# Kernel optimization log

Hardware: AMD Instinct MI355X
Metric: run time of the kernel (lower is better)

Reference implementation:

```python
import jax, jax.numpy as jnp
import numpy as np

DIM = 256
MUL = 4
NUM_ENTRIES = 64
B, K = 16, 64
R = MUL * DIM


def setup_inputs() -> dict:
    key = jax.random.key(0)
    k_slots, k_idx, k_w1, k_w2 = jax.random.split(key, 4)
    slots = jax.random.normal(k_slots, (B, K, DIM), dtype=jnp.float32)
    indices = jax.random.randint(k_idx, (B, K), 0, NUM_ENTRIES, dtype=jnp.int64)
    # xavier_normal: std = sqrt(2 / (fan_in + fan_out)) over last two dims
    std1 = float(np.sqrt(2.0 / (DIM + R)))
    std2 = float(np.sqrt(2.0 / (R + DIM)))
    w1 = jax.random.normal(k_w1, (NUM_ENTRIES, DIM, R), dtype=jnp.float32) * std1
    w2 = jax.random.normal(k_w2, (NUM_ENTRIES, R, DIM), dtype=jnp.float32) * std2
    b1 = jnp.zeros((NUM_ENTRIES, R), dtype=jnp.float32)
    b2 = jnp.zeros((NUM_ENTRIES, DIM), dtype=jnp.float32)
    return {"slots": slots, "w1": w1, "b1": b1, "w2": w2, "b2": b2, "indices": indices}


def reference(slots, w1, b1, w2, b2, indices):
    # gather per-(b,k) expert weights, then 2-layer MLP (matvec per slot)
    h = jnp.einsum('bkd,bkdr->bkr', slots, w1[indices]) + b1[indices]  # (B,K,R)
    h = jax.nn.relu(h)
    out = jnp.einsum('bkr,bkrd->bkd', h, w2[indices]) + b2[indices]    # (B,K,DIM)
    return out
```

## Files before the change

kernel.cpp:

```cpp
#include <hip/hip_runtime.h>
#include <stdint.h>

#define DIMC 256
#define RTOT 1024
#define NE 64
#define NSLOT 1024
#define RC 256
#define TILE 32
#define XSTR 264
#define KS 8
#define NTW 4

typedef short bfrag __attribute__((ext_vector_type(8)));
typedef float f32x4 __attribute__((ext_vector_type(4)));

__global__ __launch_bounds__(1024) void bucket_kernel(
    const int* __restrict__ idx, int* __restrict__ count,
    int* __restrict__ start, int* __restrict__ list) {
  __shared__ int cnt[NE];
  __shared__ int offs[NE];
  __shared__ int cur[NE];
  int t = threadIdx.x;
  if (t < NE) cnt[t] = 0;
  __syncthreads();
  int e = idx[t] & (NE - 1);
  atomicAdd(&cnt[e], 1);
  __syncthreads();
  if (t == 0) {
    int acc = 0;
    for (int i = 0; i < NE; ++i) { offs[i] = acc; cur[i] = acc; acc += cnt[i]; }
  }
  __syncthreads();
  if (t < NE) { count[t] = cnt[t]; start[t] = offs[t]; }
  int pos = atomicAdd(&cur[e], 1);
  list[pos] = t;
}

static __device__ __forceinline__ unsigned short f2bf(float f) {
  unsigned u = __float_as_uint(f);
  return (unsigned short)((u + 0x7FFFu + ((u >> 16) & 1u)) >> 16);
}

static __device__ __forceinline__ bfrag pack8(const float* f) {
  union { unsigned short u[8]; bfrag v; } r;
#pragma unroll
  for (int i = 0; i < 8; ++i) r.u[i] = f2bf(f[i]);
  return r.v;
}

__global__ __launch_bounds__(256) void mlp_kernel(
    const float* __restrict__ slots, const float* __restrict__ w1,
    const float* __restrict__ b1, const float* __restrict__ w2,
    const float* __restrict__ b2, const int* __restrict__ count,
    const int* __restrict__ start, const int* __restrict__ list,
    float* __restrict__ out) {
  const int rc = blockIdx.x;
  const int e  = blockIdx.y;
  const int n  = count[e];
  if (n == 0) return;
  const int t  = threadIdx.x;
  const int l  = t & 63;
  const int w  = t >> 6;
  const int ln = l & 15;
  const int kg = l >> 4;
  const int rbase = rc * RC;
  const int n0 = w * 64;
  const int st = start[e];

  __shared__ unsigned short X[TILE * XSTR];
  __shared__ int sid[TILE];

  const float* w1e = w1 + (size_t)e * DIMC * RTOT + rbase;
  const float* w2e = w2 + (size_t)e * RTOT * DIMC + (size_t)rbase * DIMC;

  for (int s0 = 0; s0 < n; s0 += TILE) {
    const int m = (n - s0 < TILE) ? (n - s0) : TILE;

    __syncthreads();
    if (t < TILE) sid[t] = (t < m) ? list[st + s0 + t] : 0;
    __syncthreads();

    for (int i = t; i < TILE * 64; i += 256) {
      int s = i >> 6, d4 = (i & 63) * 4;
      float4 v = make_float4(0.f, 0.f, 0.f, 0.f);
      if (s < m) v = ((const float4*)slots)[(size_t)sid[s] * 64 + (i & 63)];
      union { unsigned short u[4]; uint2 q; } p;
      p.u[0] = f2bf(v.x); p.u[1] = f2bf(v.y);
      p.u[2] = f2bf(v.z); p.u[3] = f2bf(v.w);
      *(uint2*)&X[s * XSTR + d4] = p.q;
    }
    __syncthreads();

    f32x4 acc[2][NTW];
#pragma unroll
    for (int mt = 0; mt < 2; ++mt)
#pragma unroll
      for (int nt = 0; nt < NTW; ++nt) acc[mt][nt] = (f32x4)(0.f);

    {
      float bc[NTW][8], bn[NTW][8];
#pragma unroll
      for (int nt = 0; nt < NTW; ++nt)
#pragma unroll
        for (int j = 0; j < 8; ++j)
          bc[nt][j] = w1e[(size_t)(kg * 8 + j) * RTOT + n0 + nt * 16 + ln];

#pragma unroll
      for (int ks = 0; ks < KS; ++ks) {
        if (ks + 1 < KS) {
          const int kb = (ks + 1) * 32;
#pragma unroll
          for (int nt = 0; nt < NTW; ++nt)
#pragma unroll
            for (int j = 0; j < 8; ++j)
              bn[nt][j] = w1e[(size_t)(kb + kg * 8 + j) * RTOT + n0 + nt * 16 + ln];
        }
        const unsigned short* xp = &X[(size_t)ln * XSTR + ks * 32 + kg * 8];
        bfrag a0 = *(const bfrag*)xp;
        bfrag a1 = *(const bfrag*)(xp + 16 * XSTR);
#pragma unroll
        for (int nt = 0; nt < NTW; ++nt) {
          bfrag b = pack8(bc[nt]);
          acc[0][nt] = __builtin_amdgcn_mfma_f32_16x16x32_bf16(a0, b, acc[0][nt], 0, 0, 0);
          acc[1][nt] = __builtin_amdgcn_mfma_f32_16x16x32_bf16(a1, b, acc[1][nt], 0, 0, 0);
        }
#pragma unroll
        for (int nt = 0; nt < NTW; ++nt)
#pragma unroll
          for (int j = 0; j < 8; ++j) bc[nt][j] = bn[nt][j];
      }
    }

    __syncthreads();

#pragma unroll
    for (int nt = 0; nt < NTW; ++nt) {
      const int col = n0 + nt * 16 + ln;
      const float b1v = b1[e * RTOT + rbase + col];
#pragma unroll
      for (int mt = 0; mt < 2; ++mt) {
#pragma unroll
        for (int reg = 0; reg < 4; ++reg) {
          float h = fmaxf(acc[mt][nt][reg] + b1v, 0.f);
          X[(mt * 16 + kg * 4 + reg) * XSTR + col] = f2bf(h);
        }
        acc[mt][nt] = (f32x4)(0.f);
      }
    }
    __syncthreads();

    {
      float bc[NTW][8], bn[NTW][8];
#pragma unroll
      for (int nt = 0; nt < NTW; ++nt)
#pragma unroll
        for (int j = 0; j < 8; ++j)
          bc[nt][j] = w2e[(size_t)(kg * 8 + j) * DIMC + n0 + nt * 16 + ln];

#pragma unroll
      for (int ks = 0; ks < KS; ++ks) {
        if (ks + 1 < KS) {
          const int kb = (ks + 1) * 32;
#pragma unroll
          for (int nt = 0; nt < NTW; ++nt)
#pragma unroll
            for (int j = 0; j < 8; ++j)
              bn[nt][j] = w2e[(size_t)(kb + kg * 8 + j) * DIMC + n0 + nt * 16 + ln];
        }
        const unsigned short* xp = &X[(size_t)ln * XSTR + ks * 32 + kg * 8];
        bfrag a0 = *(const bfrag*)xp;
        bfrag a1 = *(const bfrag*)(xp + 16 * XSTR);
#pragma unroll
        for (int nt = 0; nt < NTW; ++nt) {
          bfrag b = pack8(bc[nt]);
          acc[0][nt] = __builtin_amdgcn_mfma_f32_16x16x32_bf16(a0, b, acc[0][nt], 0, 0, 0);
          acc[1][nt] = __builtin_amdgcn_mfma_f32_16x16x32_bf16(a1, b, acc[1][nt], 0, 0, 0);
        }
#pragma unroll
        for (int nt = 0; nt < NTW; ++nt)
#pragma unroll
          for (int j = 0; j < 8; ++j) bc[nt][j] = bn[nt][j];
      }
    }

#pragma unroll
    for (int nt = 0; nt < NTW; ++nt) {
      const int col = n0 + nt * 16 + ln;
      const float b2v = (rc == 0) ? b2[e * DIMC + col] : 0.f;
#pragma unroll
      for (int mt = 0; mt < 2; ++mt)
#pragma unroll
        for (int reg = 0; reg < 4; ++reg) {
          const int row = mt * 16 + kg * 4 + reg;
          if (row < m)
            atomicAdd(&out[(size_t)sid[row] * DIMC + col], acc[mt][nt][reg] + b2v);
        }
    }
  }
}

extern "C" void kernel_launch(void* const* d_in, const int* in_sizes, int n_in,
                              void* d_out, int out_size, void* d_ws, size_t ws_size,
                              hipStream_t stream) {
  const float* slots   = (const float*)d_in[0];
  const float* w1      = (const float*)d_in[1];
  const float* b1      = (const float*)d_in[2];
  const float* w2      = (const float*)d_in[3];
  const float* b2      = (const float*)d_in[4];
  const int*   indices = (const int*)d_in[5];
  float* out = (float*)d_out;

  int* ws    = (int*)d_ws;
  int* count = ws;
  int* start = ws + 64;
  int* list  = ws + 128;

  hipMemsetAsync(d_out, 0, (size_t)out_size * sizeof(float), stream);
  bucket_kernel<<<1, NSLOT, 0, stream>>>(indices, count, start, list);
  mlp_kernel<<<dim3(4, NE), 256, 0, stream>>>(slots, w1, b1, w2, b2,
                                              count, start, list, out);
}
```

Measured before the change: 179.4 us.

## Split hidden dim into 8 chunks with 512-thread blocks for more parallelism

The hidden dimension is now split into 8 chunks of 128 instead of 4 chunks of 256, and each block uses 8 waves instead of 4. In the first GEMM each wave now owns one 16-column tile. In the second GEMM each wave owns 32 output columns and reduces over 128 hidden rows. This doubles the grid and the waves per block to raise occupancy and memory-level parallelism on the weight streaming, which appears to be the bottleneck. In exchange it doubles the atomicAdd traffic into the output and makes each block reload the slot tile twice as often.

```diff
diff --git a/kernel.cpp b/kernel.cpp
--- a/kernel.cpp
+++ b/kernel.cpp
@@ -5,11 +5,13 @@
 #define RTOT 1024
 #define NE 64
 #define NSLOT 1024
-#define RC 256
+#define RCN 8
+#define RCW 128
 #define TILE 32
 #define XSTR 264
-#define KS 8
-#define NTW 4
+#define KS1 8
+#define KS2 4
+#define NTW2 2
 
 typedef short bfrag __attribute__((ext_vector_type(8)));
 typedef float f32x4 __attribute__((ext_vector_type(4)));
@@ -48,7 +50,7 @@
   return r.v;
 }
 
-__global__ __launch_bounds__(256) void mlp_kernel(
+__global__ __launch_bounds__(512) void mlp_kernel(
     const float* __restrict__ slots, const float* __restrict__ w1,
     const float* __restrict__ b1, const float* __restrict__ w2,
     const float* __restrict__ b2, const int* __restrict__ count,
@@ -63,8 +65,7 @@
   const int w  = t >> 6;
   const int ln = l & 15;
   const int kg = l >> 4;
-  const int rbase = rc * RC;
-  const int n0 = w * 64;
+  const int rbase = rc * RCW;
   const int st = start[e];
 
   __shared__ unsigned short X[TILE * XSTR];
@@ -80,7 +81,7 @@
     if (t < TILE) sid[t] = (t < m) ? list[st + s0 + t] : 0;
     __syncthreads();
 
-    for (int i = t; i < TILE * 64; i += 256) {
+    for (int i = t; i < TILE * 64; i += 512) {
       int s = i >> 6, d4 = (i & 63) * 4;
       float4 v = make_float4(0.f, 0.f, 0.f, 0.f);
       if (s < m) v = ((const float4*)slots)[(size_t)sid[s] * 64 + (i & 63)];
@@ -91,101 +92,91 @@
     }
     __syncthreads();
 
-    f32x4 acc[2][NTW];
-#pragma unroll
-    for (int mt = 0; mt < 2; ++mt)
-#pragma unroll
-      for (int nt = 0; nt < NTW; ++nt) acc[mt][nt] = (f32x4)(0.f);
-
+    f32x4 acc1[2];
+    acc1[0] = (f32x4)(0.f); acc1[1] = (f32x4)(0.f);
     {
-      float bc[NTW][8], bn[NTW][8];
-#pragma unroll
-      for (int nt = 0; nt < NTW; ++nt)
-#pragma unroll
-        for (int j = 0; j < 8; ++j)
-          bc[nt][j] = w1e[(size_t)(kg * 8 + j) * RTOT + n0 + nt * 16 + ln];
-
-#pragma unroll
-      for (int ks = 0; ks < KS; ++ks) {
-        if (ks + 1 < KS) {
+      const int col = w * 16 + ln;
+      float bc[8], bn[8];
+#pragma unroll
+      for (int j = 0; j < 8; ++j)
+        bc[j] = w1e[(size_t)(kg * 8 + j) * RTOT + col];
+
+#pragma unroll
+      for (int ks = 0; ks < KS1; ++ks) {
+        if (ks + 1 < KS1) {
           const int kb = (ks + 1) * 32;
 #pragma unroll
-          for (int nt = 0; nt < NTW; ++nt)
-#pragma unroll
-            for (int j = 0; j < 8; ++j)
-              bn[nt][j] = w1e[(size_t)(kb + kg * 8 + j) * RTOT + n0 + nt * 16 + ln];
+          for (int j = 0; j < 8; ++j)
+            bn[j] = w1e[(size_t)(kb + kg * 8 + j) * RTOT + col];
         }
         const unsigned short* xp = &X[(size_t)ln * XSTR + ks * 32 + kg * 8];
         bfrag a0 = *(const bfrag*)xp;
         bfrag a1 = *(const bfrag*)(xp + 16 * XSTR);
-#pragma unroll
-        for (int nt = 0; nt < NTW; ++nt) {
-          bfrag b = pack8(bc[nt]);
-          acc[0][nt] = __builtin_amdgcn_mfma_f32_16x16x32_bf16(a0, b, acc[0][nt], 0, 0, 0);
-          acc[1][nt] = __builtin_amdgcn_mfma_f32_16x16x32_bf16(a1, b, acc[1][nt], 0, 0, 0);
-        }
-#pragma unroll
-        for (int nt = 0; nt < NTW; ++nt)
-#pragma unroll
-          for (int j = 0; j < 8; ++j) bc[nt][j] = bn[nt][j];
+        bfrag b = pack8(bc);
+        acc1[0] = __builtin_amdgcn_mfma_f32_16x16x32_bf16(a0, b, acc1[0], 0, 0, 0);
+        acc1[1] = __builtin_amdgcn_mfma_f32_16x16x32_bf16(a1, b, acc1[1], 0, 0, 0);
+#pragma unroll
+        for (int j = 0; j < 8; ++j) bc[j] = bn[j];
       }
     }
 
     __syncthreads();
 
-#pragma unroll
-    for (int nt = 0; nt < NTW; ++nt) {
-      const int col = n0 + nt * 16 + ln;
+    {
+      const int col = w * 16 + ln;
       const float b1v = b1[e * RTOT + rbase + col];
 #pragma unroll
-      for (int mt = 0; mt < 2; ++mt) {
+      for (int mt = 0; mt < 2; ++mt)
 #pragma unroll
         for (int reg = 0; reg < 4; ++reg) {
-          float h = fmaxf(acc[mt][nt][reg] + b1v, 0.f);
+          float h = fmaxf(acc1[mt][reg] + b1v, 0.f);
           X[(mt * 16 + kg * 4 + reg) * XSTR + col] = f2bf(h);
         }
-        acc[mt][nt] = (f32x4)(0.f);
-      }
-    }
-    __syncthreads();
-
+    }
+    __syncthreads();
+
+    f32x4 acc2[2][NTW2];
+#pragma unroll
+    for (int mt = 0; mt < 2; ++mt)
+#pragma unroll
+      for (int nt = 0; nt < NTW2; ++nt) acc2[mt][nt] = (f32x4)(0.f);
     {
-      float bc[NTW][8], bn[NTW][8];
-#pragma unroll
-      for (int nt = 0; nt < NTW; ++nt)
+      float bc[NTW2][8], bn[NTW2][8];
+#pragma unroll
+      for (int nt = 0; nt < NTW2; ++nt)
 #pragma unroll
         for (int j = 0; j < 8; ++j)
-          bc[nt][j] = w2e[(size_t)(kg * 8 + j) * DIMC + n0 + nt * 16 + ln];
-
-#pragma unroll
-      for (int ks = 0; ks < KS; ++ks) {
-        if (ks + 1 < KS) {
+          bc[nt][j] = w2e[(size_t)(kg * 8 + j) * DIMC + w * 32 + nt * 16 + ln];
+
+#pragma unroll
+      for (int ks = 0; ks < KS2; ++ks) {
+        if (ks + 1 < KS2) {
           const int kb = (ks + 1) * 32;
 #pragma unroll
-          for (int nt = 0; nt < NTW; ++nt)
+          for (int nt = 0; nt < NTW2; ++nt)
 #pragma unroll
             for (int j = 0; j < 8; ++j)
-              bn[nt][j] = w2e[(size_t)(kb + kg * 8 + j) * DIMC + n0 + nt * 16 + ln];
+              bn[nt][j] = w2e[(size_t)(kb + kg * 8 + j) * DIMC + w * 32 + nt * 16 + ln];
         }
         const unsigned short* xp = &X[(size_t)ln * XSTR + ks * 32 + kg * 8];
         bfrag a0 = *(const bfrag*)xp;
         bfrag a1 = *(const bfrag*)(xp + 16 * XSTR);
 #pragma unroll
-        for (int nt = 0; nt < NTW; ++nt) {
+        for (int nt = 0; nt < NTW2; ++nt) {
           bfrag b = pack8(bc[nt]);
-          acc[0][nt] = __builtin_amdgcn_mfma_f32_16x16x32_bf16(a0, b, acc[0][nt], 0, 0, 0);
-          acc[1][nt] = __builtin_amdgcn_mfma_f32_16x16x32_bf16(a1, b, acc[1][nt], 0, 0, 0);
-        }
-#pragma unroll
-        for (int nt = 0; nt < NTW; ++nt)
+          acc2[0][nt] = __builtin_amdgcn_mfma_f32_16x16x32_bf16(a0, b, acc2[0][nt], 0, 0, 0);
+          acc2[1][nt] = __builtin_amdgcn_mfma_f32_16x16x32_bf16(a1, b, acc2[1][nt], 0, 0, 0);
+        }
+#pragma unroll
+        for (int nt = 0; nt < NTW2; ++nt)
 #pragma unroll
           for (int j = 0; j < 8; ++j) bc[nt][j] = bn[nt][j];
       }
     }
 
 #pragma unroll
-    for (int nt = 0; nt < NTW; ++nt) {
-      const int col = n0 + nt * 16 + ln;
+    for (int nt = 0; nt < NTW2; ++nt) {
+      const int col = w * 32 + nt * 16 + ln;
       const float b2v = (rc == 0) ? b2[e * DIMC + col] : 0.f;
 #pragma unroll
       for (int mt = 0; mt < 2; ++mt)
@@ -193,7 +184,7 @@
         for (int reg = 0; reg < 4; ++reg) {
           const int row = mt * 16 + kg * 4 + reg;
           if (row < m)
-            atomicAdd(&out[(size_t)sid[row] * DIMC + col], acc[mt][nt][reg] + b2v);
+            atomicAdd(&out[(size_t)sid[row] * DIMC + col], acc2[mt][nt][reg] + b2v);
         }
     }
   }
@@ -217,6 +208,6 @@
 
   hipMemsetAsync(d_out, 0, (size_t)out_size * sizeof(float), stream);
   bucket_kernel<<<1, NSLOT, 0, stream>>>(indices, count, start, list);
-  mlp_kernel<<<dim3(4, NE), 256, 0, stream>>>(slots, w1, b1, w2, b2,
-                                              count, start, list, out);
-}
+  mlp_kernel<<<dim3(RCN, NE), 512, 0, stream>>>(slots, w1, b1, w2, b2,
+                                                count, start, list, out);
+}
```

New measurement: 171.4 us. 1.05x faster.
